# Kernel optimization log

Measured on AMD Instinct MI355X. Metric: run time of the kernel, lower is better.

## Reference

```python
import jax, jax.numpy as jnp
import numpy as np

N_NODES = 100000


def sage_conv(x, src, dst, counts, Wl, bl, Wr):
    # mean-aggregate source features into destination nodes
    msg_sum = jax.ops.segment_sum(x[src], dst, num_segments=N_NODES)  # [N, d]
    aggr = msg_sum / counts  # zero-degree nodes stay 0 (counts clamped to 1)
    return aggr @ Wl + bl + x @ Wr


def setup_inputs() -> dict:
    key = jax.random.key(0)
    ks = jax.random.split(key, 16)
    N, E, IN, H, OUT = N_NODES, 640000, 128, 128, 40
    x = jax.random.normal(ks[0], (N, IN), dtype=jnp.float32)
    edge_index = jax.random.randint(ks[1], (2, E), 0, N, dtype=jnp.int64)

    def lin(k, fan_in, fan_out):
        s = 1.0 / np.sqrt(fan_in)
        return jax.random.uniform(k, (fan_in, fan_out), jnp.float32, -s, s)

    return {
        "x": x,
        "edge_index": edge_index,
        "W1l": lin(ks[2], IN, H), "b1": jnp.zeros((H,), jnp.float32), "W1r": lin(ks[3], IN, H),
        "W2l": lin(ks[4], H, H), "b2": jnp.zeros((H,), jnp.float32), "W2r": lin(ks[5], H, H),
        "W3l": lin(ks[6], H, H), "b3": jnp.zeros((H,), jnp.float32), "W3r": lin(ks[7], H, H),
        "Wf1": lin(ks[8], H, H), "bf1": jnp.zeros((H,), jnp.float32),
        "Wf2": lin(ks[9], H, OUT), "bf2": jnp.zeros((OUT,), jnp.float32),
    }


def reference(x, edge_index, W1l, b1, W1r, W2l, b2, W2r, W3l, b3, W3r, Wf1, bf1, Wf2, bf2):
    src, dst = edge_index[0], edge_index[1]
    counts = jax.ops.segment_sum(jnp.ones_like(dst, dtype=x.dtype), dst,
                                 num_segments=N_NODES)
    counts = jnp.maximum(counts, 1.0)[:, None]  # [N, 1]

    h = jax.nn.relu(sage_conv(x, src, dst, counts, W1l, b1, W1r))
    h = jax.nn.relu(sage_conv(h, src, dst, counts, W2l, b2, W2r))
    h = sage_conv(h, src, dst, counts, W3l, b3, W3r)

    z = jax.nn.relu(h @ Wf1 + bf1) @ Wf2 + bf2  # [N, out]
    return jax.nn.log_softmax(z, axis=1), h
```

## Files before the change

### kernel.cpp

```cpp
#include <hip/hip_runtime.h>
#include <math.h>

#define N_NODES 100000
#define HDIM    128
#define ODIM    40
#define NBLK    ((N_NODES + 255) / 256)

typedef unsigned short u16;
typedef unsigned int   u32;
typedef short bf16x8 __attribute__((ext_vector_type(8)));
typedef float f32x4  __attribute__((ext_vector_type(4)));

__device__ inline float bf16lo_to_f(u32 v) {
    u32 u = v << 16; float f; __builtin_memcpy(&f, &u, 4); return f;
}
__device__ inline float bf16hi_to_f(u32 v) {
    u32 u = v & 0xffff0000u; float f; __builtin_memcpy(&f, &u, 4); return f;
}
__device__ inline u16 f_to_bf16(float f) {
    u32 u; __builtin_memcpy(&u, &f, 4);
    u32 r = (u + 0x7fffu + ((u >> 16) & 1u)) >> 16;
    return (u16)r;
}
__device__ inline u32 pack_bf16x2(float a, float b) {
    return (u32)f_to_bf16(a) | ((u32)f_to_bf16(b) << 16);
}

__global__ __launch_bounds__(256) void count_deg_kernel(
    const int* __restrict__ dst, int* __restrict__ ic, int E)
{
    int e = blockIdx.x * 256 + threadIdx.x;
    if (e < E) atomicAdd(ic + dst[e], 1);
}

__global__ __launch_bounds__(256) void block_sum_kernel(
    const int* __restrict__ ic, int* __restrict__ bs, int n)
{
    __shared__ int sm[256];
    int t = threadIdx.x;
    int i = blockIdx.x * 256 + t;
    sm[t] = (i < n) ? ic[i] : 0;
    __syncthreads();
    for (int s = 128; s > 0; s >>= 1) {
        if (t < s) sm[t] += sm[t + s];
        __syncthreads();
    }
    if (t == 0) bs[blockIdx.x] = sm[0];
}

__global__ __launch_bounds__(512) void scan_bs_kernel(int* __restrict__ bs, int nb)
{
    __shared__ int sm[512];
    int t = threadIdx.x;
    sm[t] = (t < nb) ? bs[t] : 0;
    __syncthreads();
    for (int off = 1; off < 512; off <<= 1) {
        int v = (t >= off) ? sm[t - off] : 0;
        __syncthreads();
        sm[t] += v;
        __syncthreads();
    }
    if (t < nb) bs[t] = (t == 0) ? 0 : sm[t - 1];
}

__global__ __launch_bounds__(256) void scan_block_kernel(
    const int* __restrict__ ic, const int* __restrict__ bs,
    int* __restrict__ pc, int n)
{
    __shared__ int sm[256];
    int t = threadIdx.x;
    int i = blockIdx.x * 256 + t;
    int v = (i < n) ? ic[i] : 0;
    sm[t] = v;
    __syncthreads();
    for (int off = 1; off < 256; off <<= 1) {
        int u = (t >= off) ? sm[t - off] : 0;
        __syncthreads();
        sm[t] += u;
        __syncthreads();
    }
    if (i < n) pc[i] = bs[blockIdx.x] + sm[t] - v;
}

__global__ __launch_bounds__(256) void fill_kernel(
    const int* __restrict__ src, const int* __restrict__ dst,
    int* __restrict__ pc, int* __restrict__ cs, int E)
{
    int e = blockIdx.x * 256 + threadIdx.x;
    if (e < E) {
        int p = atomicAdd(pc + dst[e], 1);
        cs[p] = src[e];
    }
}

__global__ __launch_bounds__(256) void f2bf_kernel(
    const float2* __restrict__ in, u32* __restrict__ out, int n2)
{
    int i = blockIdx.x * 256 + threadIdx.x;
    if (i < n2) { float2 v = in[i]; out[i] = pack_bf16x2(v.x, v.y); }
}

struct WPtrs { const float* w[7]; };

__global__ __launch_bounds__(256) void pack_w_kernel(WPtrs p, u16* __restrict__ out)
{
    int mat = blockIdx.y;
    int e = blockIdx.x * 256 + threadIdx.x;
    int k = e >> 7, n = e & 127;
    float v = p.w[mat][e];
    int nt = n >> 4, ks = k >> 5, q = (k >> 3) & 3, j = k & 7;
    int dst = mat * 16384 + (((nt * 4 + ks) * 64 + q * 16 + (n & 15)) << 3) + j;
    out[dst] = f_to_bf16(v);
}

__global__ __launch_bounds__(256) void pack_wf2_kernel(
    const float* __restrict__ Wf2, u16* __restrict__ outp)
{
    int e = blockIdx.x * 256 + threadIdx.x;
    if (e >= 128 * 48) return;
    int k = e / 48, n = e - k * 48;
    float v = (n < ODIM) ? Wf2[k * ODIM + n] : 0.f;
    int nt = n >> 4, ks = k >> 5, q = (k >> 3) & 3, j = k & 7;
    outp[(((nt * 4 + ks) * 64 + q * 16 + (n & 15)) << 3) + j] = f_to_bf16(v);
}

__global__ __launch_bounds__(256) void gather_mean_grp_kernel(
    const u32* __restrict__ feat,
    const int* __restrict__ cs, const int* __restrict__ pc, const int* __restrict__ ic,
    u32* __restrict__ A)
{
    const int grp  = threadIdx.x >> 4;
    const int ch   = threadIdx.x & 15;
    const int node = blockIdx.x * 16 + grp;
    const int end  = pc[node];
    const int deg  = ic[node];
    const int start = end - deg;

    const u32* fb = feat + (ch << 2);

    float acc[8] = {0.f,0.f,0.f,0.f,0.f,0.f,0.f,0.f};
    const uint4 Z = {0u, 0u, 0u, 0u};

    if (deg > 0) {
        uint4 c0 = *reinterpret_cast<const uint4*>(fb + ((size_t)cs[start] << 6));
        uint4 c1 = (deg > 1)
            ? *reinterpret_cast<const uint4*>(fb + ((size_t)cs[start + 1] << 6)) : Z;
        for (int j = 0; j < deg; ++j) {
            uint4 n = (j + 2 < deg)
                ? *reinterpret_cast<const uint4*>(fb + ((size_t)cs[start + j + 2] << 6)) : Z;
            acc[0] += bf16lo_to_f(c0.x); acc[1] += bf16hi_to_f(c0.x);
            acc[2] += bf16lo_to_f(c0.y); acc[3] += bf16hi_to_f(c0.y);
            acc[4] += bf16lo_to_f(c0.z); acc[5] += bf16hi_to_f(c0.z);
            acc[6] += bf16lo_to_f(c0.w); acc[7] += bf16hi_to_f(c0.w);
            c0 = c1; c1 = n;
        }
    }

    float inv = 1.0f / (float)(deg > 0 ? deg : 1);
    uint4 o;
    o.x = pack_bf16x2(acc[0] * inv, acc[1] * inv);
    o.y = pack_bf16x2(acc[2] * inv, acc[3] * inv);
    o.z = pack_bf16x2(acc[4] * inv, acc[5] * inv);
    o.w = pack_bf16x2(acc[6] * inv, acc[7] * inv);
    *reinterpret_cast<uint4*>(A + ((size_t)node << 6) + (ch << 2)) = o;
}

__global__ __launch_bounds__(256) void mfma_gemm_kernel(
    const u16* __restrict__ A1, const u16* __restrict__ A2,
    const u16* __restrict__ W1p, const u16* __restrict__ W2p,
    const float* __restrict__ bias,
    u16* __restrict__ out16, float* __restrict__ out32, int do_relu)
{
    __shared__ __align__(16) u16 sBuf[128 * 136];
    const int tid  = threadIdx.x;
    const int wave = tid >> 6;
    const int lane = tid & 63;
    const int m = lane & 15;
    const int q = lane >> 4;
    const int base = blockIdx.x * 128;

    int row0 = base + wave * 16 + m;        if (row0 > N_NODES - 1) row0 = N_NODES - 1;
    int row1 = base + (wave + 4) * 16 + m;  if (row1 > N_NODES - 1) row1 = N_NODES - 1;

    f32x4 acc0[8], acc1[8];
    #pragma unroll
    for (int nt = 0; nt < 8; ++nt) {
        acc0[nt] = (f32x4){0.f, 0.f, 0.f, 0.f};
        acc1[nt] = (f32x4){0.f, 0.f, 0.f, 0.f};
    }

    bf16x8 a0[4], a1[4];
    #pragma unroll
    for (int ks = 0; ks < 4; ++ks) {
        a0[ks] = *reinterpret_cast<const bf16x8*>(A1 + ((size_t)row0 << 7) + ((ks * 4 + q) << 3));
        a1[ks] = *reinterpret_cast<const bf16x8*>(A1 + ((size_t)row1 << 7) + ((ks * 4 + q) << 3));
    }
    #pragma unroll
    for (int it = 0; it < 8; ++it) {
        int off = (it * 4 + wave) << 9;
        __builtin_amdgcn_global_load_lds(
            (const __attribute__((address_space(1))) void*)(W1p + off + (lane << 3)),
            (__attribute__((address_space(3))) void*)(sBuf + off), 16, 0, 0);
    }
    __syncthreads();

    #pragma unroll
    for (int ks = 0; ks < 4; ++ks) {
        #pragma unroll
        for (int nt = 0; nt < 8; ++nt) {
            bf16x8 b = *reinterpret_cast<const bf16x8*>(sBuf + (((nt * 4 + ks) * 64 + lane) << 3));
            acc0[nt] = __builtin_amdgcn_mfma_f32_16x16x32_bf16(a0[ks], b, acc0[nt], 0, 0, 0);
            acc1[nt] = __builtin_amdgcn_mfma_f32_16x16x32_bf16(a1[ks], b, acc1[nt], 0, 0, 0);
        }
    }

    if (A2 != nullptr) {
        __syncthreads();
        #pragma unroll
        for (int ks = 0; ks < 4; ++ks) {
            a0[ks] = *reinterpret_cast<const bf16x8*>(A2 + ((size_t)row0 << 7) + ((ks * 4 + q) << 3));
            a1[ks] = *reinterpret_cast<const bf16x8*>(A2 + ((size_t)row1 << 7) + ((ks * 4 + q) << 3));
        }
        #pragma unroll
        for (int it = 0; it < 8; ++it) {
            int off = (it * 4 + wave) << 9;
            __builtin_amdgcn_global_load_lds(
                (const __attribute__((address_space(1))) void*)(W2p + off + (lane << 3)),
                (__attribute__((address_space(3))) void*)(sBuf + off), 16, 0, 0);
        }
        __syncthreads();

        #pragma unroll
        for (int ks = 0; ks < 4; ++ks) {
            #pragma unroll
            for (int nt = 0; nt < 8; ++nt) {
                bf16x8 b = *reinterpret_cast<const bf16x8*>(sBuf + (((nt * 4 + ks) * 64 + lane) << 3));
                acc0[nt] = __builtin_amdgcn_mfma_f32_16x16x32_bf16(a0[ks], b, acc0[nt], 0, 0, 0);
                acc1[nt] = __builtin_amdgcn_mfma_f32_16x16x32_bf16(a1[ks], b, acc1[nt], 0, 0, 0);
            }
        }
    }
    __syncthreads();

    #pragma unroll
    for (int nt = 0; nt < 8; ++nt) {
        int col = nt * 16 + m;
        float bv = bias[col];
        #pragma unroll
        for (int r = 0; r < 4; ++r) {
            float v0 = acc0[nt][r] + bv;
            float v1 = acc1[nt][r] + bv;
            if (do_relu) { v0 = fmaxf(v0, 0.f); v1 = fmaxf(v1, 0.f); }
            int rl0 = wave * 16 + q * 4 + r;
            int rl1 = rl0 + 64;
            sBuf[rl0 * 136 + col] = f_to_bf16(v0);
            sBuf[rl1 * 136 + col] = f_to_bf16(v1);
            if (out32) {
                int rg0 = base + rl0, rg1 = base + rl1;
                if (rg0 < N_NODES) out32[((size_t)rg0 << 7) + col] = v0;
                if (rg1 < N_NODES) out32[((size_t)rg1 << 7) + col] = v1;
            }
        }
    }
    __syncthreads();

    if (out16) {
        #pragma unroll
        for (int it = 0; it < 8; ++it) {
            int c = it * 256 + tid;
            int row = c >> 4, ch = c & 15;
            int rowg = base + row;
            if (rowg < N_NODES)
                *reinterpret_cast<uint4*>(out16 + ((size_t)rowg << 7) + (ch << 3)) =
                    *reinterpret_cast<const uint4*>(sBuf + row * 136 + (ch << 3));
        }
    }
}

__global__ __launch_bounds__(256) void mfma_head_kernel(
    const u16* __restrict__ h3,
    const u16* __restrict__ Wf1p, const float* __restrict__ bf1,
    const u16* __restrict__ Wf2p, const float* __restrict__ bf2,
    float* __restrict__ out)
{
    __shared__ __align__(16) u16 sW1[16384];
    __shared__ __align__(16) u16 sW2[6144];
    const int tid  = threadIdx.x;
    const int base = blockIdx.x * 64;
    const int wave = tid >> 6;
    const int lane = tid & 63;
    const int m = lane & 15;
    const int q = lane >> 4;

    int row = base + wave * 16 + m; if (row > N_NODES - 1) row = N_NODES - 1;

    bf16x8 a[4];
    #pragma unroll
    for (int ks = 0; ks < 4; ++ks)
        a[ks] = *reinterpret_cast<const bf16x8*>(h3 + ((size_t)row << 7) + ((ks * 4 + q) << 3));

    #pragma unroll
    for (int it = 0; it < 8; ++it) {
        int off = (it * 4 + wave) << 9;
        __builtin_amdgcn_global_load_lds(
            (const __attribute__((address_space(1))) void*)(Wf1p + off + (lane << 3)),
            (__attribute__((address_space(3))) void*)(sW1 + off), 16, 0, 0);
    }
    #pragma unroll
    for (int it = 0; it < 3; ++it) {
        int off = (it * 4 + wave) << 9;
        __builtin_amdgcn_global_load_lds(
            (const __attribute__((address_space(1))) void*)(Wf2p + off + (lane << 3)),
            (__attribute__((address_space(3))) void*)(sW2 + off), 16, 0, 0);
    }
    __syncthreads();

    f32x4 acc[8];
    #pragma unroll
    for (int nt = 0; nt < 8; ++nt) acc[nt] = (f32x4){0.f, 0.f, 0.f, 0.f};
    #pragma unroll
    for (int ks = 0; ks < 4; ++ks) {
        #pragma unroll
        for (int nt = 0; nt < 8; ++nt) {
            bf16x8 b = *reinterpret_cast<const bf16x8*>(sW1 + (((nt * 4 + ks) * 64 + lane) << 3));
            acc[nt] = __builtin_amdgcn_mfma_f32_16x16x32_bf16(a[ks], b, acc[nt], 0, 0, 0);
        }
    }
    __syncthreads();

    #pragma unroll
    for (int nt = 0; nt < 8; ++nt) {
        int col = nt * 16 + m;
        float bv = bf1[col];
        #pragma unroll
        for (int r = 0; r < 4; ++r) {
            float v = fmaxf(acc[nt][r] + bv, 0.f);
            int dc = (wave * 4 + (nt >> 1)) * 64 + ((nt & 1) * 2 + (m >> 3)) * 16 + (q * 4 + r);
            sW1[(dc << 3) | (m & 7)] = f_to_bf16(v);
        }
    }
    __syncthreads();

    f32x4 acc2[3];
    #pragma unroll
    for (int nt = 0; nt < 3; ++nt) acc2[nt] = (f32x4){0.f, 0.f, 0.f, 0.f};
    #pragma unroll
    for (int ks = 0; ks < 4; ++ks) {
        bf16x8 a2 = *reinterpret_cast<const bf16x8*>(sW1 + (((wave * 4 + ks) * 64 + lane) << 3));
        #pragma unroll
        for (int nt = 0; nt < 3; ++nt) {
            bf16x8 b = *reinterpret_cast<const bf16x8*>(sW2 + (((nt * 4 + ks) * 64 + lane) << 3));
            acc2[nt] = __builtin_amdgcn_mfma_f32_16x16x32_bf16(a2, b, acc2[nt], 0, 0, 0);
        }
    }

    float z[3][4];
    float mx[4] = {-INFINITY, -INFINITY, -INFINITY, -INFINITY};
    #pragma unroll
    for (int nt = 0; nt < 3; ++nt) {
        int col = nt * 16 + m;
        bool valid = (col < ODIM);
        float bv = valid ? bf2[col] : 0.f;
        #pragma unroll
        for (int r = 0; r < 4; ++r) {
            z[nt][r] = acc2[nt][r] + bv;
            if (valid) mx[r] = fmaxf(mx[r], z[nt][r]);
        }
    }
    #pragma unroll
    for (int off = 1; off < 16; off <<= 1) {
        #pragma unroll
        for (int r = 0; r < 4; ++r) mx[r] = fmaxf(mx[r], __shfl_xor(mx[r], off, 16));
    }
    float sum[4] = {0.f, 0.f, 0.f, 0.f};
    #pragma unroll
    for (int nt = 0; nt < 3; ++nt) {
        int col = nt * 16 + m;
        if (col < ODIM) {
            #pragma unroll
            for (int r = 0; r < 4; ++r) sum[r] += expf(z[nt][r] - mx[r]);
        }
    }
    #pragma unroll
    for (int off = 1; off < 16; off <<= 1) {
        #pragma unroll
        for (int r = 0; r < 4; ++r) sum[r] += __shfl_xor(sum[r], off, 16);
    }
    float lse[4];
    #pragma unroll
    for (int r = 0; r < 4; ++r) lse[r] = logf(sum[r]) + mx[r];

    #pragma unroll
    for (int nt = 0; nt < 3; ++nt) {
        int col = nt * 16 + m;
        if (col >= ODIM) continue;
        #pragma unroll
        for (int r = 0; r < 4; ++r) {
            int rowg = base + wave * 16 + q * 4 + r;
            if (rowg >= N_NODES) continue;
            out[(size_t)rowg * ODIM + col] = z[nt][r] - lse[r];
        }
    }
}

extern "C" void kernel_launch(void* const* d_in, const int* in_sizes, int n_in,
                              void* d_out, int out_size, void* d_ws, size_t ws_size,
                              hipStream_t stream) {
    const float* x   = (const float*)d_in[0];
    const int*   ei  = (const int*)d_in[1];
    const int E = in_sizes[1] / 2;
    const int* src = ei;
    const int* dst = ei + E;

    const float* W1l = (const float*)d_in[2];
    const float* b1  = (const float*)d_in[3];
    const float* W1r = (const float*)d_in[4];
    const float* W2l = (const float*)d_in[5];
    const float* b2  = (const float*)d_in[6];
    const float* W2r = (const float*)d_in[7];
    const float* W3l = (const float*)d_in[8];
    const float* b3  = (const float*)d_in[9];
    const float* W3r = (const float*)d_in[10];
    const float* Wf1 = (const float*)d_in[11];
    const float* bf1 = (const float*)d_in[12];
    const float* Wf2 = (const float*)d_in[13];
    const float* bf2 = (const float*)d_in[14];

    float* out     = (float*)d_out;
    float* outTail = out + (size_t)N_NODES * ODIM;

    int* ic = (int*)out;
    int* pc = ic + 100352;
    int* bs = pc + 100352;
    int* cs = bs + 1024;

    const size_t FEAT16 = (size_t)N_NODES * HDIM;
    u16* X16  = (u16*)d_ws;
    u16* F16a = X16  + FEAT16;
    u16* F16b = F16a + FEAT16;
    u16* A16  = F16b + FEAT16;
    u16* Wpk  = A16  + FEAT16;
    u16* Wp_1l = Wpk + 0 * 16384;
    u16* Wp_1r = Wpk + 1 * 16384;
    u16* Wp_2l = Wpk + 2 * 16384;
    u16* Wp_2r = Wpk + 3 * 16384;
    u16* Wp_3l = Wpk + 4 * 16384;
    u16* Wp_3r = Wpk + 5 * 16384;
    u16* Wp_f1 = Wpk + 6 * 16384;
    u16* Wf2p  = Wpk + 7 * 16384;

    const int gemmGrid   = (N_NODES + 127) / 128;
    const int headGrid   = (N_NODES + 63) / 64;
    const int gatherGrid = N_NODES / 16;
    const int edgeGrid   = (E + 255) / 256;
    const int cvtGrid    = (N_NODES * HDIM / 2 + 255) / 256;

    hipMemsetAsync(ic, 0, N_NODES * sizeof(int), stream);
    count_deg_kernel<<<edgeGrid, 256, 0, stream>>>(dst, ic, E);
    block_sum_kernel<<<NBLK, 256, 0, stream>>>(ic, bs, N_NODES);
    scan_bs_kernel<<<1, 512, 0, stream>>>(bs, NBLK);
    scan_block_kernel<<<NBLK, 256, 0, stream>>>(ic, bs, pc, N_NODES);
    fill_kernel<<<edgeGrid, 256, 0, stream>>>(src, dst, pc, cs, E);

    f2bf_kernel<<<cvtGrid, 256, 0, stream>>>((const float2*)x, (u32*)X16, N_NODES * HDIM / 2);
    WPtrs wp; wp.w[0] = W1l; wp.w[1] = W1r; wp.w[2] = W2l; wp.w[3] = W2r;
    wp.w[4] = W3l; wp.w[5] = W3r; wp.w[6] = Wf1;
    pack_w_kernel<<<dim3(64, 7), 256, 0, stream>>>(wp, Wpk);
    pack_wf2_kernel<<<24, 256, 0, stream>>>(Wf2, Wf2p);

    gather_mean_grp_kernel<<<gatherGrid, 256, 0, stream>>>((const u32*)X16, cs, pc, ic, (u32*)A16);
    mfma_gemm_kernel<<<gemmGrid, 256, 0, stream>>>(A16, X16, Wp_1l, Wp_1r, b1, F16a, nullptr, 1);

    gather_mean_grp_kernel<<<gatherGrid, 256, 0, stream>>>((const u32*)F16a, cs, pc, ic, (u32*)A16);
    mfma_gemm_kernel<<<gemmGrid, 256, 0, stream>>>(A16, F16a, Wp_2l, Wp_2r, b2, F16b, nullptr, 1);

    gather_mean_grp_kernel<<<gatherGrid, 256, 0, stream>>>((const u32*)F16b, cs, pc, ic, (u32*)A16);
    mfma_gemm_kernel<<<gemmGrid, 256, 0, stream>>>(A16, F16b, Wp_3l, Wp_3r, b3, F16a, outTail, 0);

    mfma_head_kernel<<<headGrid, 256, 0, stream>>>(F16a, Wp_f1, bf1, Wf2p, bf2, out);
}
```

Baseline: 402.1 us.

## Fuse neighbor mean-gather into layer GEMM and fuse layer three with head

Each SAGE layer now gathers and averages neighbor features directly into shared memory inside the GEMM kernel. This removes the intermediate aggregate buffer write/read and a separate launch. The third layer also runs the MLP head and log-softmax in the same kernel, avoiding the h3 re-read. In exchange, each block gathers 128 nodes in 8 sequential batches with fewer blocks, which may reduce latency hiding for the irregular gather. The CSR scratch buffers also move from the output buffer to the workspace.

```diff
diff --git a/kernel.cpp b/kernel.cpp
--- a/kernel.cpp
+++ b/kernel.cpp
@@ -124,52 +124,116 @@
     outp[(((nt * 4 + ks) * 64 + q * 16 + (n & 15)) << 3) + j] = f_to_bf16(v);
 }
 
-__global__ __launch_bounds__(256) void gather_mean_grp_kernel(
-    const u32* __restrict__ feat,
+__device__ inline void gather_phase(
+    const u32* __restrict__ feat32, const int* __restrict__ cs,
+    const int* __restrict__ pc, const int* __restrict__ ic,
+    u16* __restrict__ sBuf, int base, int tid)
+{
+    const int grp = tid >> 4;
+    const int ch  = tid & 15;
+    const u32* fb = feat32 + (ch << 2);
+    const uint4 Z = {0u, 0u, 0u, 0u};
+
+    for (int b = 0; b < 8; ++b) {
+        int rl = b * 16 + grp;
+        int node = base + rl;
+        int deg = 0, start = 0;
+        if (node < N_NODES) { int e = pc[node]; deg = ic[node]; start = e - deg; }
+
+        float acc[8] = {0.f,0.f,0.f,0.f,0.f,0.f,0.f,0.f};
+        if (deg > 0) {
+            uint4 c0 = *reinterpret_cast<const uint4*>(fb + ((size_t)cs[start] << 6));
+            uint4 c1 = (deg > 1)
+                ? *reinterpret_cast<const uint4*>(fb + ((size_t)cs[start + 1] << 6)) : Z;
+            for (int j = 0; j < deg; ++j) {
+                uint4 nx = (j + 2 < deg)
+                    ? *reinterpret_cast<const uint4*>(fb + ((size_t)cs[start + j + 2] << 6)) : Z;
+                acc[0] += bf16lo_to_f(c0.x); acc[1] += bf16hi_to_f(c0.x);
+                acc[2] += bf16lo_to_f(c0.y); acc[3] += bf16hi_to_f(c0.y);
+                acc[4] += bf16lo_to_f(c0.z); acc[5] += bf16hi_to_f(c0.z);
+                acc[6] += bf16lo_to_f(c0.w); acc[7] += bf16hi_to_f(c0.w);
+                c0 = c1; c1 = nx;
+            }
+        }
+        float inv = 1.0f / (float)(deg > 0 ? deg : 1);
+        uint4 o;
+        o.x = pack_bf16x2(acc[0] * inv, acc[1] * inv);
+        o.y = pack_bf16x2(acc[2] * inv, acc[3] * inv);
+        o.z = pack_bf16x2(acc[4] * inv, acc[5] * inv);
+        o.w = pack_bf16x2(acc[6] * inv, acc[7] * inv);
+        *reinterpret_cast<uint4*>(sBuf + rl * 136 + (ch << 3)) = o;
+    }
+}
+
+__device__ inline void stage_w(const u16* __restrict__ Wp, u16* __restrict__ sDst,
+                               int wave, int lane, int nchunk4)
+{
+    for (int it = 0; it < nchunk4; ++it) {
+        int off = (it * 4 + wave) << 9;
+        __builtin_amdgcn_global_load_lds(
+            (const __attribute__((address_space(1))) void*)(Wp + off + (lane << 3)),
+            (__attribute__((address_space(3))) void*)(sDst + off), 16, 0, 0);
+    }
+}
+
+__device__ inline void head_softmax_store(
+    const f32x4* acc2, const float* __restrict__ bf2, float* __restrict__ out,
+    int rowbase, int m, int q)
+{
+    float z[3][4];
+    float mx[4] = {-INFINITY, -INFINITY, -INFINITY, -INFINITY};
+    #pragma unroll
+    for (int nt = 0; nt < 3; ++nt) {
+        int col = nt * 16 + m;
+        bool valid = (col < ODIM);
+        float bv = valid ? bf2[col] : 0.f;
+        #pragma unroll
+        for (int r = 0; r < 4; ++r) {
+            z[nt][r] = acc2[nt][r] + bv;
+            if (valid) mx[r] = fmaxf(mx[r], z[nt][r]);
+        }
+    }
+    #pragma unroll
+    for (int off = 1; off < 16; off <<= 1) {
+        #pragma unroll
+        for (int r = 0; r < 4; ++r) mx[r] = fmaxf(mx[r], __shfl_xor(mx[r], off, 16));
+    }
+    float sum[4] = {0.f, 0.f, 0.f, 0.f};
+    #pragma unroll
+    for (int nt = 0; nt < 3; ++nt) {
+        int col = nt * 16 + m;
+        if (col < ODIM) {
+            #pragma unroll
+            for (int r = 0; r < 4; ++r) sum[r] += expf(z[nt][r] - mx[r]);
+        }
+    }
+    #pragma unroll
+    for (int off = 1; off < 16; off <<= 1) {
+        #pragma unroll
+        for (int r = 0; r < 4; ++r) sum[r] += __shfl_xor(sum[r], off, 16);
+    }
+    float lse[4];
+    #pragma unroll
+    for (int r = 0; r < 4; ++r) lse[r] = logf(sum[r]) + mx[r];
+
+    #pragma unroll
+    for (int nt = 0; nt < 3; ++nt) {
+        int col = nt * 16 + m;
+        if (col >= ODIM) continue;
+        #pragma unroll
+        for (int r = 0; r < 4; ++r) {
+            int rowg = rowbase + q * 4 + r;
+            if (rowg < N_NODES) out[(size_t)rowg * ODIM + col] = z[nt][r] - lse[r];
+        }
+    }
+}
+
+__global__ __launch_bounds__(256) void sage_layer_kernel(
+    const u16* __restrict__ feat,
     const int* __restrict__ cs, const int* __restrict__ pc, const int* __restrict__ ic,
-    u32* __restrict__ A)
-{
-    const int grp  = threadIdx.x >> 4;
-    const int ch   = threadIdx.x & 15;
-    const int node = blockIdx.x * 16 + grp;
-    const int end  = pc[node];
-    const int deg  = ic[node];
-    const int start = end - deg;
-
-    const u32* fb = feat + (ch << 2);
-
-    float acc[8] = {0.f,0.f,0.f,0.f,0.f,0.f,0.f,0.f};
-    const uint4 Z = {0u, 0u, 0u, 0u};
-
-    if (deg > 0) {
-        uint4 c0 = *reinterpret_cast<const uint4*>(fb + ((size_t)cs[start] << 6));
-        uint4 c1 = (deg > 1)
-            ? *reinterpret_cast<const uint4*>(fb + ((size_t)cs[start + 1] << 6)) : Z;
-        for (int j = 0; j < deg; ++j) {
-            uint4 n = (j + 2 < deg)
-                ? *reinterpret_cast<const uint4*>(fb + ((size_t)cs[start + j + 2] << 6)) : Z;
-            acc[0] += bf16lo_to_f(c0.x); acc[1] += bf16hi_to_f(c0.x);
-            acc[2] += bf16lo_to_f(c0.y); acc[3] += bf16hi_to_f(c0.y);
-            acc[4] += bf16lo_to_f(c0.z); acc[5] += bf16hi_to_f(c0.z);
-            acc[6] += bf16lo_to_f(c0.w); acc[7] += bf16hi_to_f(c0.w);
-            c0 = c1; c1 = n;
-        }
-    }
-
-    float inv = 1.0f / (float)(deg > 0 ? deg : 1);
-    uint4 o;
-    o.x = pack_bf16x2(acc[0] * inv, acc[1] * inv);
-    o.y = pack_bf16x2(acc[2] * inv, acc[3] * inv);
-    o.z = pack_bf16x2(acc[4] * inv, acc[5] * inv);
-    o.w = pack_bf16x2(acc[6] * inv, acc[7] * inv);
-    *reinterpret_cast<uint4*>(A + ((size_t)node << 6) + (ch << 2)) = o;
-}
-
-__global__ __launch_bounds__(256) void mfma_gemm_kernel(
-    const u16* __restrict__ A1, const u16* __restrict__ A2,
-    const u16* __restrict__ W1p, const u16* __restrict__ W2p,
+    const u16* __restrict__ Wlp, const u16* __restrict__ Wrp,
     const float* __restrict__ bias,
-    u16* __restrict__ out16, float* __restrict__ out32, int do_relu)
+    u16* __restrict__ out16)
 {
     __shared__ __align__(16) u16 sBuf[128 * 136];
     const int tid  = threadIdx.x;
@@ -179,8 +243,27 @@
     const int q = lane >> 4;
     const int base = blockIdx.x * 128;
 
-    int row0 = base + wave * 16 + m;        if (row0 > N_NODES - 1) row0 = N_NODES - 1;
-    int row1 = base + (wave + 4) * 16 + m;  if (row1 > N_NODES - 1) row1 = N_NODES - 1;
+    gather_phase((const u32*)feat, cs, pc, ic, sBuf, base, tid);
+    __syncthreads();
+
+    const int rl0 = wave * 16 + m;
+    const int rl1 = rl0 + 64;
+    bf16x8 g0[4], g1[4];
+    #pragma unroll
+    for (int ks = 0; ks < 4; ++ks) {
+        g0[ks] = *reinterpret_cast<const bf16x8*>(sBuf + rl0 * 136 + ((ks * 4 + q) << 3));
+        g1[ks] = *reinterpret_cast<const bf16x8*>(sBuf + rl1 * 136 + ((ks * 4 + q) << 3));
+    }
+    __syncthreads();
+
+    int row0 = base + rl0; if (row0 > N_NODES - 1) row0 = N_NODES - 1;
+    int row1 = base + rl1; if (row1 > N_NODES - 1) row1 = N_NODES - 1;
+    bf16x8 s0[4], s1[4];
+    #pragma unroll
+    for (int ks = 0; ks < 4; ++ks) {
+        s0[ks] = *reinterpret_cast<const bf16x8*>(feat + ((size_t)row0 << 7) + ((ks * 4 + q) << 3));
+        s1[ks] = *reinterpret_cast<const bf16x8*>(feat + ((size_t)row1 << 7) + ((ks * 4 + q) << 3));
+    }
 
     f32x4 acc0[8], acc1[8];
     #pragma unroll
@@ -189,55 +272,28 @@
         acc1[nt] = (f32x4){0.f, 0.f, 0.f, 0.f};
     }
 
-    bf16x8 a0[4], a1[4];
-    #pragma unroll
-    for (int ks = 0; ks < 4; ++ks) {
-        a0[ks] = *reinterpret_cast<const bf16x8*>(A1 + ((size_t)row0 << 7) + ((ks * 4 + q) << 3));
-        a1[ks] = *reinterpret_cast<const bf16x8*>(A1 + ((size_t)row1 << 7) + ((ks * 4 + q) << 3));
-    }
-    #pragma unroll
-    for (int it = 0; it < 8; ++it) {
-        int off = (it * 4 + wave) << 9;
-        __builtin_amdgcn_global_load_lds(
-            (const __attribute__((address_space(1))) void*)(W1p + off + (lane << 3)),
-            (__attribute__((address_space(3))) void*)(sBuf + off), 16, 0, 0);
-    }
-    __syncthreads();
-
+    stage_w(Wlp, sBuf, wave, lane, 8);
+    __syncthreads();
     #pragma unroll
     for (int ks = 0; ks < 4; ++ks) {
         #pragma unroll
         for (int nt = 0; nt < 8; ++nt) {
             bf16x8 b = *reinterpret_cast<const bf16x8*>(sBuf + (((nt * 4 + ks) * 64 + lane) << 3));
-            acc0[nt] = __builtin_amdgcn_mfma_f32_16x16x32_bf16(a0[ks], b, acc0[nt], 0, 0, 0);
-            acc1[nt] = __builtin_amdgcn_mfma_f32_16x16x32_bf16(a1[ks], b, acc1[nt], 0, 0, 0);
-        }
-    }
-
-    if (A2 != nullptr) {
-        __syncthreads();
-        #pragma unroll
-        for (int ks = 0; ks < 4; ++ks) {
-            a0[ks] = *reinterpret_cast<const bf16x8*>(A2 + ((size_t)row0 << 7) + ((ks * 4 + q) << 3));
-            a1[ks] = *reinterpret_cast<const bf16x8*>(A2 + ((size_t)row1 << 7) + ((ks * 4 + q) << 3));
-        }
-        #pragma unroll
-        for (int it = 0; it < 8; ++it) {
-            int off = (it * 4 + wave) << 9;
-            __builtin_amdgcn_global_load_lds(
-                (const __attribute__((address_space(1))) void*)(W2p + off + (lane << 3)),
-                (__attribute__((address_space(3))) void*)(sBuf + off), 16, 0, 0);
-        }
-        __syncthreads();
-
-        #pragma unroll
-        for (int ks = 0; ks < 4; ++ks) {
-            #pragma unroll
-            for (int nt = 0; nt < 8; ++nt) {
-                bf16x8 b = *reinterpret_cast<const bf16x8*>(sBuf + (((nt * 4 + ks) * 64 + lane) << 3));
-                acc0[nt] = __builtin_amdgcn_mfma_f32_16x16x32_bf16(a0[ks], b, acc0[nt], 0, 0, 0);
-                acc1[nt] = __builtin_amdgcn_mfma_f32_16x16x32_bf16(a1[ks], b, acc1[nt], 0, 0, 0);
-            }
+            acc0[nt] = __builtin_amdgcn_mfma_f32_16x16x32_bf16(g0[ks], b, acc0[nt], 0, 0, 0);
+            acc1[nt] = __builtin_amdgcn_mfma_f32_16x16x32_bf16(g1[ks], b, acc1[nt], 0, 0, 0);
+        }
+    }
+    __syncthreads();
+
+    stage_w(Wrp, sBuf, wave, lane, 8);
+    __syncthreads();
+    #pragma unroll
+    for (int ks = 0; ks < 4; ++ks) {
+        #pragma unroll
+        for (int nt = 0; nt < 8; ++nt) {
+            bf16x8 b = *reinterpret_cast<const bf16x8*>(sBuf + (((nt * 4 + ks) * 64 + lane) << 3));
+            acc0[nt] = __builtin_amdgcn_mfma_f32_16x16x32_bf16(s0[ks], b, acc0[nt], 0, 0, 0);
+            acc1[nt] = __builtin_amdgcn_mfma_f32_16x16x32_bf16(s1[ks], b, acc1[nt], 0, 0, 0);
         }
     }
     __syncthreads();
@@ -248,82 +304,138 @@
         float bv = bias[col];
         #pragma unroll
         for (int r = 0; r < 4; ++r) {
-            float v0 = acc0[nt][r] + bv;
-            float v1 = acc1[nt][r] + bv;
-            if (do_relu) { v0 = fmaxf(v0, 0.f); v1 = fmaxf(v1, 0.f); }
-            int rl0 = wave * 16 + q * 4 + r;
-            int rl1 = rl0 + 64;
-            sBuf[rl0 * 136 + col] = f_to_bf16(v0);
-            sBuf[rl1 * 136 + col] = f_to_bf16(v1);
-            if (out32) {
-                int rg0 = base + rl0, rg1 = base + rl1;
-                if (rg0 < N_NODES) out32[((size_t)rg0 << 7) + col] = v0;
-                if (rg1 < N_NODES) out32[((size_t)rg1 << 7) + col] = v1;
-            }
-        }
-    }
-    __syncthreads();
-
-    if (out16) {
-        #pragma unroll
-        for (int it = 0; it < 8; ++it) {
-            int c = it * 256 + tid;
-            int row = c >> 4, ch = c & 15;
-            int rowg = base + row;
-            if (rowg < N_NODES)
-                *reinterpret_cast<uint4*>(out16 + ((size_t)rowg << 7) + (ch << 3)) =
-                    *reinterpret_cast<const uint4*>(sBuf + row * 136 + (ch << 3));
-        }
-    }
-}
-
-__global__ __launch_bounds__(256) void mfma_head_kernel(
-    const u16* __restrict__ h3,
+            float v0 = fmaxf(acc0[nt][r] + bv, 0.f);
+            float v1 = fmaxf(acc1[nt][r] + bv, 0.f);
+            int rlr = wave * 16 + q * 4 + r;
+            sBuf[rlr * 136 + col] = f_to_bf16(v0);
+            sBuf[(rlr + 64) * 136 + col] = f_to_bf16(v1);
+        }
+    }
+    __syncthreads();
+
+    #pragma unroll
+    for (int it = 0; it < 8; ++it) {
+        int c = it * 256 + tid;
+        int row = c >> 4, ch = c & 15;
+        int rowg = base + row;
+        if (rowg < N_NODES)
+            *reinterpret_cast<uint4*>(out16 + ((size_t)rowg << 7) + (ch << 3)) =
+                *reinterpret_cast<const uint4*>(sBuf + row * 136 + (ch << 3));
+    }
+}
+
+__global__ __launch_bounds__(256) void sage_l3_head_kernel(
+    const u16* __restrict__ feat,
+    const int* __restrict__ cs, const int* __restrict__ pc, const int* __restrict__ ic,
+    const u16* __restrict__ W3lp, const u16* __restrict__ W3rp,
+    const float* __restrict__ b3,
     const u16* __restrict__ Wf1p, const float* __restrict__ bf1,
     const u16* __restrict__ Wf2p, const float* __restrict__ bf2,
+    float* __restrict__ hout,
     float* __restrict__ out)
 {
-    __shared__ __align__(16) u16 sW1[16384];
-    __shared__ __align__(16) u16 sW2[6144];
+    __shared__ __align__(16) u16 sBuf[128 * 136];
     const int tid  = threadIdx.x;
-    const int base = blockIdx.x * 64;
     const int wave = tid >> 6;
     const int lane = tid & 63;
     const int m = lane & 15;
     const int q = lane >> 4;
-
-    int row = base + wave * 16 + m; if (row > N_NODES - 1) row = N_NODES - 1;
-
-    bf16x8 a[4];
-    #pragma unroll
-    for (int ks = 0; ks < 4; ++ks)
-        a[ks] = *reinterpret_cast<const bf16x8*>(h3 + ((size_t)row << 7) + ((ks * 4 + q) << 3));
-
-    #pragma unroll
-    for (int it = 0; it < 8; ++it) {
-        int off = (it * 4 + wave) << 9;
-        __builtin_amdgcn_global_load_lds(
-            (const __attribute__((address_space(1))) void*)(Wf1p + off + (lane << 3)),
-            (__attribute__((address_space(3))) void*)(sW1 + off), 16, 0, 0);
-    }
-    #pragma unroll
-    for (int it = 0; it < 3; ++it) {
-        int off = (it * 4 + wave) << 9;
-        __builtin_amdgcn_global_load_lds(
-            (const __attribute__((address_space(1))) void*)(Wf2p + off + (lane << 3)),
-            (__attribute__((address_space(3))) void*)(sW2 + off), 16, 0, 0);
-    }
-    __syncthreads();
-
-    f32x4 acc[8];
-    #pragma unroll
-    for (int nt = 0; nt < 8; ++nt) acc[nt] = (f32x4){0.f, 0.f, 0.f, 0.f};
+    const int base = blockIdx.x * 128;
+
+    gather_phase((const u32*)feat, cs, pc, ic, sBuf, base, tid);
+    __syncthreads();
+
+    const int rl0 = wave * 16 + m;
+    const int rl1 = rl0 + 64;
+    bf16x8 g0[4], g1[4];
+    #pragma unroll
+    for (int ks = 0; ks < 4; ++ks) {
+        g0[ks] = *reinterpret_cast<const bf16x8*>(sBuf + rl0 * 136 + ((ks * 4 + q) << 3));
+        g1[ks] = *reinterpret_cast<const bf16x8*>(sBuf + rl1 * 136 + ((ks * 4 + q) << 3));
+    }
+    __syncthreads();
+
+    int row0 = base + rl0; if (row0 > N_NODES - 1) row0 = N_NODES - 1;
+    int row1 = base + rl1; if (row1 > N_NODES - 1) row1 = N_NODES - 1;
+    bf16x8 s0[4], s1[4];
+    #pragma unroll
+    for (int ks = 0; ks < 4; ++ks) {
+        s0[ks] = *reinterpret_cast<const bf16x8*>(feat + ((size_t)row0 << 7) + ((ks * 4 + q) << 3));
+        s1[ks] = *reinterpret_cast<const bf16x8*>(feat + ((size_t)row1 << 7) + ((ks * 4 + q) << 3));
+    }
+
+    f32x4 acc0[8], acc1[8];
+    #pragma unroll
+    for (int nt = 0; nt < 8; ++nt) {
+        acc0[nt] = (f32x4){0.f, 0.f, 0.f, 0.f};
+        acc1[nt] = (f32x4){0.f, 0.f, 0.f, 0.f};
+    }
+
+    stage_w(W3lp, sBuf, wave, lane, 8);
+    __syncthreads();
     #pragma unroll
     for (int ks = 0; ks < 4; ++ks) {
         #pragma unroll
         for (int nt = 0; nt < 8; ++nt) {
-            bf16x8 b = *reinterpret_cast<const bf16x8*>(sW1 + (((nt * 4 + ks) * 64 + lane) << 3));
-            acc[nt] = __builtin_amdgcn_mfma_f32_16x16x32_bf16(a[ks], b, acc[nt], 0, 0, 0);
+            bf16x8 b = *reinterpret_cast<const bf16x8*>(sBuf + (((nt * 4 + ks) * 64 + lane) << 3));
+            acc0[nt] = __builtin_amdgcn_mfma_f32_16x16x32_bf16(g0[ks], b, acc0[nt], 0, 0, 0);
+            acc1[nt] = __builtin_amdgcn_mfma_f32_16x16x32_bf16(g1[ks], b, acc1[nt], 0, 0, 0);
+        }
+    }
+    __syncthreads();
+    stage_w(W3rp, sBuf, wave, lane, 8);
+    __syncthreads();
+    #pragma unroll
+    for (int ks = 0; ks < 4; ++ks) {
+        #pragma unroll
+        for (int nt = 0; nt < 8; ++nt) {
+            bf16x8 b = *reinterpret_cast<const bf16x8*>(sBuf + (((nt * 4 + ks) * 64 + lane) << 3));
+            acc0[nt] = __builtin_amdgcn_mfma_f32_16x16x32_bf16(s0[ks], b, acc0[nt], 0, 0, 0);
+            acc1[nt] = __builtin_amdgcn_mfma_f32_16x16x32_bf16(s1[ks], b, acc1[nt], 0, 0, 0);
+        }
+    }
+    __syncthreads();
+
+    #pragma unroll
+    for (int nt = 0; nt < 8; ++nt) {
+        int col = nt * 16 + m;
+        float bv = b3[col];
+        #pragma unroll
+        for (int r = 0; r < 4; ++r) {
+            float v0 = acc0[nt][r] + bv;
+            float v1 = acc1[nt][r] + bv;
+            int rlr = wave * 16 + q * 4 + r;
+            sBuf[rlr * 136 + col] = f_to_bf16(v0);
+            sBuf[(rlr + 64) * 136 + col] = f_to_bf16(v1);
+            int rg0 = base + rlr, rg1 = base + rlr + 64;
+            if (rg0 < N_NODES) hout[((size_t)rg0 << 7) + col] = v0;
+            if (rg1 < N_NODES) hout[((size_t)rg1 << 7) + col] = v1;
+        }
+    }
+    __syncthreads();
+
+    bf16x8 h0[4], h1[4];
+    #pragma unroll
+    for (int ks = 0; ks < 4; ++ks) {
+        h0[ks] = *reinterpret_cast<const bf16x8*>(sBuf + rl0 * 136 + ((ks * 4 + q) << 3));
+        h1[ks] = *reinterpret_cast<const bf16x8*>(sBuf + rl1 * 136 + ((ks * 4 + q) << 3));
+    }
+    __syncthreads();
+
+    stage_w(Wf1p, sBuf, wave, lane, 8);
+    __syncthreads();
+    #pragma unroll
+    for (int nt = 0; nt < 8; ++nt) {
+        acc0[nt] = (f32x4){0.f, 0.f, 0.f, 0.f};
+        acc1[nt] = (f32x4){0.f, 0.f, 0.f, 0.f};
+    }
+    #pragma unroll
+    for (int ks = 0; ks < 4; ++ks) {
+        #pragma unroll
+        for (int nt = 0; nt < 8; ++nt) {
+            bf16x8 b = *reinterpret_cast<const bf16x8*>(sBuf + (((nt * 4 + ks) * 64 + lane) << 3));
+            acc0[nt] = __builtin_amdgcn_mfma_f32_16x16x32_bf16(h0[ks], b, acc0[nt], 0, 0, 0);
+            acc1[nt] = __builtin_amdgcn_mfma_f32_16x16x32_bf16(h1[ks], b, acc1[nt], 0, 0, 0);
         }
     }
     __syncthreads();
@@ -334,73 +446,41 @@
         float bv = bf1[col];
         #pragma unroll
         for (int r = 0; r < 4; ++r) {
-            float v = fmaxf(acc[nt][r] + bv, 0.f);
-            int dc = (wave * 4 + (nt >> 1)) * 64 + ((nt & 1) * 2 + (m >> 3)) * 16 + (q * 4 + r);
-            sW1[(dc << 3) | (m & 7)] = f_to_bf16(v);
-        }
-    }
-    __syncthreads();
-
-    f32x4 acc2[3];
-    #pragma unroll
-    for (int nt = 0; nt < 3; ++nt) acc2[nt] = (f32x4){0.f, 0.f, 0.f, 0.f};
-    #pragma unroll
-    for (int ks = 0; ks < 4; ++ks) {
-        bf16x8 a2 = *reinterpret_cast<const bf16x8*>(sW1 + (((wave * 4 + ks) * 64 + lane) << 3));
+            int rlr = wave * 16 + q * 4 + r;
+            sBuf[rlr * 136 + col] = f_to_bf16(fmaxf(acc0[nt][r] + bv, 0.f));
+            sBuf[(rlr + 64) * 136 + col] = f_to_bf16(fmaxf(acc1[nt][r] + bv, 0.f));
+        }
+    }
+    __syncthreads();
+
+    bf16x8 t0[4], t1[4];
+    #pragma unroll
+    for (int ks = 0; ks < 4; ++ks) {
+        t0[ks] = *reinterpret_cast<const bf16x8*>(sBuf + rl0 * 136 + ((ks * 4 + q) << 3));
+        t1[ks] = *reinterpret_cast<const bf16x8*>(sBuf + rl1 * 136 + ((ks * 4 + q) << 3));
+    }
+    __syncthreads();
+
+    stage_w(Wf2p, sBuf, wave, lane, 3);
+    __syncthreads();
+    f32x4 ca[3], cb[3];
+    #pragma unroll
+    for (int nt = 0; nt < 3; ++nt) {
+        ca[nt] = (f32x4){0.f, 0.f, 0.f, 0.f};
+        cb[nt] = (f32x4){0.f, 0.f, 0.f, 0.f};
+    }
+    #pragma unroll
+    for (int ks = 0; ks < 4; ++ks) {
         #pragma unroll
         for (int nt = 0; nt < 3; ++nt) {
-            bf16x8 b = *reinterpret_cast<const bf16x8*>(sW2 + (((nt * 4 + ks) * 64 + lane) << 3));
-            acc2[nt] = __builtin_amdgcn_mfma_f32_16x16x32_bf16(a2, b, acc2[nt], 0, 0, 0);
-        }
-    }
-
-    float z[3][4];
-    float mx[4] = {-INFINITY, -INFINITY, -INFINITY, -INFINITY};
-    #pragma unroll
-    for (int nt = 0; nt < 3; ++nt) {
-        int col = nt * 16 + m;
-        bool valid = (col < ODIM);
-        float bv = valid ? bf2[col] : 0.f;
-        #pragma unroll
-        for (int r = 0; r < 4; ++r) {
-            z[nt][r] = acc2[nt][r] + bv;
-            if (valid) mx[r] = fmaxf(mx[r], z[nt][r]);
-        }
-    }
-    #pragma unroll
-    for (int off = 1; off < 16; off <<= 1) {
-        #pragma unroll
-        for (int r = 0; r < 4; ++r) mx[r] = fmaxf(mx[r], __shfl_xor(mx[r], off, 16));
-    }
-    float sum[4] = {0.f, 0.f, 0.f, 0.f};
-    #pragma unroll
-    for (int nt = 0; nt < 3; ++nt) {
-        int col = nt * 16 + m;
-        if (col < ODIM) {
-            #pragma unroll
-            for (int r = 0; r < 4; ++r) sum[r] += expf(z[nt][r] - mx[r]);
-        }
-    }
-    #pragma unroll
-    for (int off = 1; off < 16; off <<= 1) {
-        #pragma unroll
-        for (int r = 0; r < 4; ++r) sum[r] += __shfl_xor(sum[r], off, 16);
-    }
-    float lse[4];
-    #pragma unroll
-    for (int r = 0; r < 4; ++r) lse[r] = logf(sum[r]) + mx[r];
-
-    #pragma unroll
-    for (int nt = 0; nt < 3; ++nt) {
-        int col = nt * 16 + m;
-        if (col >= ODIM) continue;
-        #pragma unroll
-        for (int r = 0; r < 4; ++r) {
-            int rowg = base + wave * 16 + q * 4 + r;
-            if (rowg >= N_NODES) continue;
-            out[(size_t)rowg * ODIM + col] = z[nt][r] - lse[r];
-        }
-    }
+            bf16x8 b = *reinterpret_cast<const bf16x8*>(sBuf + (((nt * 4 + ks) * 64 + lane) << 3));
+            ca[nt] = __builtin_amdgcn_mfma_f32_16x16x32_bf16(t0[ks], b, ca[nt], 0, 0, 0);
+            cb[nt] = __builtin_amdgcn_mfma_f32_16x16x32_bf16(t1[ks], b, cb[nt], 0, 0, 0);
+        }
+    }
+
+    head_softmax_store(ca, bf2, out, base + wave * 16, m, q);
+    head_softmax_store(cb, bf2, out, base + 64 + wave * 16, m, q);
 }
 
 extern "C" void kernel_launch(void* const* d_in, const int* in_sizes, int n_in,
@@ -429,17 +509,15 @@
     float* out     = (float*)d_out;
     float* outTail = out + (size_t)N_NODES * ODIM;
 
-    int* ic = (int*)out;
-    int* pc = ic + 100352;
-    int* bs = pc + 100352;
-    int* cs = bs + 1024;
-
     const size_t FEAT16 = (size_t)N_NODES * HDIM;
     u16* X16  = (u16*)d_ws;
     u16* F16a = X16  + FEAT16;
     u16* F16b = F16a + FEAT16;
-    u16* A16  = F16b + FEAT16;
-    u16* Wpk  = A16  + FEAT16;
+    int* ic = (int*)(F16b + FEAT16);
+    int* pc = ic + 100352;
+    int* bs = pc + 100352;
+    int* cs = bs + 1024;
+    u16* Wpk  = X16 + 4 * FEAT16;
     u16* Wp_1l = Wpk + 0 * 16384;
     u16* Wp_1r = Wpk + 1 * 16384;
     u16* Wp_2l = Wpk + 2 * 16384;
@@ -449,9 +527,7 @@
     u16* Wp_f1 = Wpk + 6 * 16384;
     u16* Wf2p  = Wpk + 7 * 16384;
 
-    const int gemmGrid   = (N_NODES + 127) / 128;
-    const int headGrid   = (N_NODES + 63) / 64;
-    const int gatherGrid = N_NODES / 16;
+    const int layerGrid  = (N_NODES + 127) / 128;
     const int edgeGrid   = (E + 255) / 256;
     const int cvtGrid    = (N_NODES * HDIM / 2 + 255) / 256;
 
@@ -468,14 +544,12 @@
     pack_w_kernel<<<dim3(64, 7), 256, 0, stream>>>(wp, Wpk);
     pack_wf2_kernel<<<24, 256, 0, stream>>>(Wf2, Wf2p);
 
-    gather_mean_grp_kernel<<<gatherGrid, 256, 0, stream>>>((const u32*)X16, cs, pc, ic, (u32*)A16);
-    mfma_gemm_kernel<<<gemmGrid, 256, 0, stream>>>(A16, X16, Wp_1l, Wp_1r, b1, F16a, nullptr, 1);
-
-    gather_mean_grp_kernel<<<gatherGrid, 256, 0, stream>>>((const u32*)F16a, cs, pc, ic, (u32*)A16);
-    mfma_gemm_kernel<<<gemmGrid, 256, 0, stream>>>(A16, F16a, Wp_2l, Wp_2r, b2, F16b, nullptr, 1);
-
-    gather_mean_grp_kernel<<<gatherGrid, 256, 0, stream>>>((const u32*)F16b, cs, pc, ic, (u32*)A16);
-    mfma_gemm_kernel<<<gemmGrid, 256, 0, stream>>>(A16, F16b, Wp_3l, Wp_3r, b3, F16a, outTail, 0);
-
-    mfma_head_kernel<<<headGrid, 256, 0, stream>>>(F16a, Wp_f1, bf1, Wf2p, bf2, out);
-}
+    sage_layer_kernel<<<layerGrid, 256, 0, stream>>>(
+        X16, cs, pc, ic, Wp_1l, Wp_1r, b1, F16a);
+
+    sage_layer_kernel<<<layerGrid, 256, 0, stream>>>(
+        F16a, cs, pc, ic, Wp_2l, Wp_2r, b2, F16b);
+
+    sage_l3_head_kernel<<<layerGrid, 256, 0, stream>>>(
+        F16b, cs, pc, ic, Wp_3l, Wp_3r, b3, Wp_f1, bf1, Wf2p, bf2, outTail, out);
+}
```

Measured after the change: 547.7 us. +36.2%, slower.
